# Kernel optimization log

Hardware: AMD Instinct MI355X
Metric: run time of the kernel (lower is better)

The kernel has to match this reference:

```python
import jax, jax.numpy as jnp
import numpy as np

EPS = 1e-8
N_ITERS = 3
LN_EPS = 1e-5  # torch LayerNorm default


def layer_norm(x, g, b):
    mu = jnp.mean(x, axis=-1, keepdims=True)
    var = jnp.var(x, axis=-1, keepdims=True)
    return (x - mu) / jnp.sqrt(var + LN_EPS) * g + b


def setup_inputs() -> dict:
    key = jax.random.key(0)
    ks = jax.random.split(key, 12)
    B, S, F, D_in, D_slot, D_kvq, D_hid = 64, 16, 4096, 512, 512, 512, 2048
    p = lambda i, shape: jax.random.normal(ks[i], shape, dtype=jnp.float32) * 0.02
    return dict(
        slots=jax.random.normal(ks[0], (B, S, D_slot), dtype=jnp.float32),
        features=jax.random.normal(ks[1], (B, F, D_in), dtype=jnp.float32),
        ln_feat_g=jnp.ones((D_in,), jnp.float32), ln_feat_b=jnp.zeros((D_in,), jnp.float32),
        ln_slot_g=jnp.ones((D_slot,), jnp.float32), ln_slot_b=jnp.zeros((D_slot,), jnp.float32),
        w_k=p(2, (D_kvq, D_in)), w_v=p(3, (D_kvq, D_in)), w_q=p(4, (D_kvq, D_slot)),
        gru_w_ih=p(5, (3 * D_slot, D_kvq)), gru_w_hh=p(6, (3 * D_slot, D_slot)),
        gru_b_ih=jnp.zeros((3 * D_slot,), jnp.float32), gru_b_hh=jnp.zeros((3 * D_slot,), jnp.float32),
        mlp_ln_g=jnp.ones((D_slot,), jnp.float32), mlp_ln_b=jnp.zeros((D_slot,), jnp.float32),
        mlp_w1=p(7, (D_hid, D_slot)), mlp_b1=jnp.zeros((D_hid,), jnp.float32),
        mlp_w2=p(8, (D_slot, D_hid)), mlp_b2=jnp.zeros((D_slot,), jnp.float32),
    )


def reference(slots, features, ln_feat_g, ln_feat_b, ln_slot_g, ln_slot_b,
              w_k, w_v, w_q, gru_w_ih, gru_w_hh, gru_b_ih, gru_b_hh,
              mlp_ln_g, mlp_ln_b, mlp_w1, mlp_b1, mlp_w2, mlp_b2):
    scale = w_q.shape[0] ** -0.5  # kvq_dim**-0.5

    f = layer_norm(features, ln_feat_g, ln_feat_b)  # [B,F,D_in]
    keys = f @ w_k.T    # [B,F,D_kvq]
    values = f @ w_v.T  # [B,F,D_kvq]

    def gru_cell(x, h):  # torch.nn.GRUCell semantics
        gi = x @ gru_w_ih.T + gru_b_ih
        gh = h @ gru_w_hh.T + gru_b_hh
        i_r, i_z, i_n = jnp.split(gi, 3, axis=-1)
        h_r, h_z, h_n = jnp.split(gh, 3, axis=-1)
        r = jax.nn.sigmoid(i_r + h_r)
        z = jax.nn.sigmoid(i_z + h_z)
        n = jnp.tanh(i_n + r * h_n)
        return (1.0 - z) * n + z * h

    pre_norm_attn = None
    for _ in range(N_ITERS):  # fixed small iteration count (n_iters=3)
        s_n = layer_norm(slots, ln_slot_g, ln_slot_b)  # note: GRU hidden uses normed slots, per source
        q = s_n @ w_q.T                                 # [B,S,D_kvq]
        dots = jnp.einsum('bsd,bfd->bsf', q, keys) * scale
        pre_norm_attn = jax.nn.softmax(dots, axis=1)    # softmax over SLOT dim
        attn = pre_norm_attn + EPS
        attn = attn / jnp.sum(attn, axis=-1, keepdims=True)
        updates = jnp.einsum('bsf,bfd->bsd', attn, values)
        slots = gru_cell(updates, s_n)
        # residual MLP with initial LayerNorm
        h = layer_norm(slots, mlp_ln_g, mlp_ln_b)
        h = jax.nn.relu(h @ mlp_w1.T + mlp_b1) @ mlp_w2.T + mlp_b2
        slots = slots + h
    return slots, pre_norm_attn
```

## Files before the change

### kernel.cpp

```cpp
#include <hip/hip_runtime.h>


typedef __bf16 bf16x8 __attribute__((ext_vector_type(8)));
typedef float  f32x4  __attribute__((ext_vector_type(4)));

#define DEV static __device__ __forceinline__

DEV float bf2f_lo(unsigned int u) { union { unsigned int i; float f; } v; v.i = u << 16; return v.f; }
DEV unsigned short f2bf(float f) {
  union { float f; unsigned int i; } v; v.f = f;
  return (unsigned short)((v.i + 0x7FFFu + ((v.i >> 16) & 1u)) >> 16);
}

template<int OUTF>
__global__ __launch_bounds__(256) void ln512_kernel(
    const float* __restrict__ X, const float* __restrict__ g,
    const float* __restrict__ b, unsigned short* __restrict__ Yb,
    float* __restrict__ Yf, int R) {
  int wave = (blockIdx.x << 2) | (threadIdx.x >> 6);
  int lane = threadIdx.x & 63;
  if (wave >= R) return;
  const float4* xp = reinterpret_cast<const float4*>(X + (size_t)wave * 512);
  float4 x0 = xp[lane * 2], x1 = xp[lane * 2 + 1];
  float xv[8] = {x0.x, x0.y, x0.z, x0.w, x1.x, x1.y, x1.z, x1.w};
  float s = 0.f, q = 0.f;
#pragma unroll
  for (int j = 0; j < 8; ++j) { s += xv[j]; q += xv[j] * xv[j]; }
#pragma unroll
  for (int off = 32; off; off >>= 1) { s += __shfl_xor(s, off); q += __shfl_xor(q, off); }
  float mu = s * (1.0f / 512.0f);
  float var = q * (1.0f / 512.0f) - mu * mu;
  float rstd = rsqrtf(var + 1e-5f);
  const float4* gp = reinterpret_cast<const float4*>(g);
  const float4* bp = reinterpret_cast<const float4*>(b);
  float4 g0 = gp[lane * 2], g1 = gp[lane * 2 + 1];
  float4 b0 = bp[lane * 2], b1 = bp[lane * 2 + 1];
  float gv[8] = {g0.x, g0.y, g0.z, g0.w, g1.x, g1.y, g1.z, g1.w};
  float bv[8] = {b0.x, b0.y, b0.z, b0.w, b1.x, b1.y, b1.z, b1.w};
  float y[8];
  unsigned short u[8];
#pragma unroll
  for (int j = 0; j < 8; ++j) { y[j] = (xv[j] - mu) * rstd * gv[j] + bv[j]; u[j] = f2bf(y[j]); }
  uint4 o = make_uint4(
      (unsigned)u[0] | ((unsigned)u[1] << 16), (unsigned)u[2] | ((unsigned)u[3] << 16),
      (unsigned)u[4] | ((unsigned)u[5] << 16), (unsigned)u[6] | ((unsigned)u[7] << 16));
  reinterpret_cast<uint4*>(Yb + (size_t)wave * 512)[lane] = o;
  if (OUTF) {
    float4* yf = reinterpret_cast<float4*>(Yf + (size_t)wave * 512);
    yf[lane * 2]     = make_float4(y[0], y[1], y[2], y[3]);
    yf[lane * 2 + 1] = make_float4(y[4], y[5], y[6], y[7]);
  }
}

__global__ __launch_bounds__(256) void prep_weights_kernel(
    const float* __restrict__ w_ih, const float* __restrict__ w_hh,
    const float* __restrict__ w1, const float* __restrict__ w2,
    const float* __restrict__ w_k, const float* __restrict__ w_q,
    const float* __restrict__ w_v,
    unsigned short* __restrict__ Wih, unsigned short* __restrict__ Whh,
    unsigned short* __restrict__ W1, unsigned short* __restrict__ W2,
    unsigned short* __restrict__ WkT, unsigned short* __restrict__ WqT,
    unsigned short* __restrict__ WvT) {
  int blk = blockIdx.x, tid = threadIdx.x;
  if (blk < 3584) {
    const float* src; unsigned short* dst; int base;
    if (blk < 768)       { src = w_ih; dst = Wih; base = blk; }
    else if (blk < 1536) { src = w_hh; dst = Whh; base = blk - 768; }
    else if (blk < 2560) { src = w1;   dst = W1;  base = blk - 1536; }
    else                 { src = w2;   dst = W2;  base = blk - 2560; }
    int i = base * 256 + tid;
    float4 v = reinterpret_cast<const float4*>(src)[i];
    unsigned int lo = (unsigned)f2bf(v.x) | ((unsigned)f2bf(v.y) << 16);
    unsigned int hi = (unsigned)f2bf(v.z) | ((unsigned)f2bf(v.w) << 16);
    reinterpret_cast<uint2*>(dst)[i] = make_uint2(lo, hi);
  } else {
    int rgn = (blk - 3584) >> 10, base = (blk - 3584) & 1023;
    const float* src = rgn == 0 ? w_k : rgn == 1 ? w_q : w_v;
    unsigned short* dst = rgn == 0 ? WkT : rgn == 1 ? WqT : WvT;
    int t2 = base * 256 + tid;
    int i = t2 >> 9, j = t2 & 511;
    dst[t2] = f2bf(src[j * 512 + i]);
  }
}

template<int MODE>
__global__ __launch_bounds__(256) void gemm_nt(
    const unsigned short* __restrict__ A, const unsigned short* __restrict__ Bm,
    const float* __restrict__ bias, unsigned short* __restrict__ Cb,
    int M, int N, int K) {
  int lane = threadIdx.x & 63;
  int w = threadIdx.x >> 6;
  int m0 = blockIdx.y << 5;
  int n0 = (blockIdx.x << 7) + (w << 5);
  int lo = lane & 15, hi = lane >> 4;
  const unsigned short* Ap = A + (size_t)(m0 + lo) * K + (hi << 3);
  const unsigned short* Bp = Bm + (size_t)(n0 + lo) * K + (hi << 3);
  f32x4 acc[2][2];
#pragma unroll
  for (int i = 0; i < 2; ++i)
#pragma unroll
    for (int j = 0; j < 2; ++j) acc[i][j] = f32x4{0.f, 0.f, 0.f, 0.f};
#pragma unroll 2
  for (int kk = 0; kk < K; kk += 32) {
    bf16x8 a0 = *reinterpret_cast<const bf16x8*>(Ap + kk);
    bf16x8 a1 = *reinterpret_cast<const bf16x8*>(Ap + (size_t)16 * K + kk);
    bf16x8 b0 = *reinterpret_cast<const bf16x8*>(Bp + kk);
    bf16x8 b1 = *reinterpret_cast<const bf16x8*>(Bp + (size_t)16 * K + kk);
    acc[0][0] = __builtin_amdgcn_mfma_f32_16x16x32_bf16(a0, b0, acc[0][0], 0, 0, 0);
    acc[0][1] = __builtin_amdgcn_mfma_f32_16x16x32_bf16(a0, b1, acc[0][1], 0, 0, 0);
    acc[1][0] = __builtin_amdgcn_mfma_f32_16x16x32_bf16(a1, b0, acc[1][0], 0, 0, 0);
    acc[1][1] = __builtin_amdgcn_mfma_f32_16x16x32_bf16(a1, b1, acc[1][1], 0, 0, 0);
  }
#pragma unroll
  for (int i = 0; i < 2; ++i)
#pragma unroll
    for (int j = 0; j < 2; ++j) {
      int col = n0 + (j << 4) + lo;
      float bvv = (MODE == 3) ? bias[col] : 0.f;
#pragma unroll
      for (int r = 0; r < 4; ++r) {
        int row = m0 + (i << 4) + (hi << 2) + r;
        float v = acc[i][j][r];
        if (MODE == 0) Cb[(size_t)row * N + col] = f2bf(v);
        else           Cb[(size_t)row * N + col] = f2bf(fmaxf(v + bvv, 0.f));
      }
    }
}

template<int MODE>
__global__ __launch_bounds__(256) void gemm_nt64(
    const unsigned short* __restrict__ A, const unsigned short* __restrict__ Bm,
    const float* __restrict__ bias, const float* __restrict__ res,
    float* __restrict__ Cf, unsigned short* __restrict__ Cb,
    int M, int N, int K) {
  int lane = threadIdx.x & 63;
  int w = threadIdx.x >> 6;
  int m0 = (blockIdx.y << 5) + ((w >> 1) << 4);
  int n0 = (blockIdx.x << 6) + ((w & 1) << 5);
  int lo = lane & 15, hi = lane >> 4;
  const unsigned short* Ap = A + (size_t)(m0 + lo) * K + (hi << 3);
  const unsigned short* Bp = Bm + (size_t)(n0 + lo) * K + (hi << 3);
  f32x4 acc[2];
  acc[0] = f32x4{0.f, 0.f, 0.f, 0.f};
  acc[1] = f32x4{0.f, 0.f, 0.f, 0.f};
#pragma unroll 2
  for (int kk = 0; kk < K; kk += 32) {
    bf16x8 a0 = *reinterpret_cast<const bf16x8*>(Ap + kk);
    bf16x8 b0 = *reinterpret_cast<const bf16x8*>(Bp + kk);
    bf16x8 b1 = *reinterpret_cast<const bf16x8*>(Bp + (size_t)16 * K + kk);
    acc[0] = __builtin_amdgcn_mfma_f32_16x16x32_bf16(a0, b0, acc[0], 0, 0, 0);
    acc[1] = __builtin_amdgcn_mfma_f32_16x16x32_bf16(a0, b1, acc[1], 0, 0, 0);
  }
#pragma unroll
  for (int j = 0; j < 2; ++j) {
    int col = n0 + (j << 4) + lo;
    float bvv = (MODE == 4) ? bias[col] : 0.f;
#pragma unroll
    for (int r = 0; r < 4; ++r) {
      int row = m0 + (hi << 2) + r;
      float v = acc[j][r];
      if (MODE == 0) Cb[(size_t)row * N + col] = f2bf(v);
      else Cf[(size_t)row * N + col] = v + bvv + res[(size_t)row * N + col];
    }
  }
}

__global__ __launch_bounds__(128) void fused_attn_kernel(
    const unsigned short* __restrict__ Qp,
    const unsigned short* __restrict__ Fn,
    float* __restrict__ Upart,
    float* __restrict__ fsumP,
    float* __restrict__ attn_out) {
  __shared__ unsigned short tile[32 * 514];
  __shared__ unsigned short attn_lds[16 * 34];
  int b = blockIdx.y, g = blockIdx.x;
  int t = threadIdx.x;
  int w = t >> 6, lane = t & 63;
  int lo = lane & 15, hi = lane >> 4;
  unsigned int* tile32 = reinterpret_cast<unsigned int*>(tile);

  const unsigned short* qa = Qp + ((size_t)b * 16 + lo) * 512 + (hi << 3);
  const unsigned short* gstage = Fn + ((size_t)b * 4096 + g * 256) * 512;

  f32x4 uacc[16];
#pragma unroll
  for (int s = 0; s < 16; ++s) uacc[s] = f32x4{0.f, 0.f, 0.f, 0.f};
  float fs[4] = {0.f, 0.f, 0.f, 0.f};

  const float scale = 0.04419417382415922f;

  {
    uint4 nx[16];
#pragma unroll
    for (int k = 0; k < 16; ++k)
      nx[k] = *reinterpret_cast<const uint4*>(gstage + (size_t)t * 8 + k * 1024);
#pragma unroll
    for (int k = 0; k < 16; ++k) {
      unsigned int* p32 = tile32 + (k * 2 + w) * 257 + lane * 4;
      p32[0] = nx[k].x; p32[1] = nx[k].y; p32[2] = nx[k].z; p32[3] = nx[k].w;
    }
  }
  __syncthreads();

  for (int c = 0; c < 8; ++c) {
    uint4 nx[16];
    if (c < 7) {
      const unsigned short* src = gstage + (size_t)(c + 1) * 16384;
#pragma unroll
      for (int k = 0; k < 16; ++k)
        nx[k] = *reinterpret_cast<const uint4*>(src + (size_t)t * 8 + k * 1024);
    }
    f32x4 dacc = {0.f, 0.f, 0.f, 0.f};
#pragma unroll
    for (int ks = 0; ks < 16; ++ks) {
      const unsigned int* bp32 = tile32 + (w * 16 + lo) * 257 + ks * 16 + (hi << 2);
      union { unsigned int u[4]; bf16x8 v; } bf;
      bf.u[0] = bp32[0]; bf.u[1] = bp32[1]; bf.u[2] = bp32[2]; bf.u[3] = bp32[3];
      bf16x8 a = *reinterpret_cast<const bf16x8*>(qa + ks * 32);
      dacc = __builtin_amdgcn_mfma_f32_16x16x32_bf16(a, bf.v, dacc, 0, 0, 0);
    }
    float d4[4], mx = -3.4e38f;
#pragma unroll
    for (int r = 0; r < 4; ++r) { d4[r] = dacc[r] * scale; mx = fmaxf(mx, d4[r]); }
    mx = fmaxf(mx, __shfl_xor(mx, 16));
    mx = fmaxf(mx, __shfl_xor(mx, 32));
    float e4[4], ss = 0.f;
#pragma unroll
    for (int r = 0; r < 4; ++r) { e4[r] = __expf(d4[r] - mx); ss += e4[r]; }
    ss += __shfl_xor(ss, 16);
    ss += __shfl_xor(ss, 32);
    float inv = 1.f / ss;
    float cs[4];
#pragma unroll
    for (int r = 0; r < 4; ++r) {
      float p = e4[r] * inv;
      if (attn_out)
        attn_out[((size_t)b * 16 + (hi << 2) + r) * 4096 + g * 256 + c * 32 + (w << 4) + lo] = p;
      unsigned short uu = f2bf(p + 1e-8f);
      attn_lds[((hi << 2) + r) * 34 + (w << 4) + lo] = uu;
      cs[r] = bf2f_lo(uu);
    }
#pragma unroll
    for (int m = 1; m < 16; m <<= 1) {
#pragma unroll
      for (int r = 0; r < 4; ++r) cs[r] += __shfl_xor(cs[r], m);
    }
#pragma unroll
    for (int r = 0; r < 4; ++r) fs[r] += cs[r];
    __syncthreads();
    {
      const unsigned int* ap32 = reinterpret_cast<const unsigned int*>(attn_lds) + lo * 17 + (hi << 2);
      union { unsigned int u[4]; bf16x8 v; } paf;
      paf.u[0] = ap32[0]; paf.u[1] = ap32[1]; paf.u[2] = ap32[2]; paf.u[3] = ap32[3];
#pragma unroll
      for (int sub = 0; sub < 16; ++sub) {
        int dcol = (w << 8) + (sub << 4) + lo;
        union { unsigned short u[8]; bf16x8 v; } pbf;
#pragma unroll
        for (int j = 0; j < 8; ++j)
          pbf.u[j] = tile[((hi << 3) + j) * 514 + dcol];
        uacc[sub] = __builtin_amdgcn_mfma_f32_16x16x32_bf16(paf.v, pbf.v, uacc[sub], 0, 0, 0);
      }
    }
    __syncthreads();
    if (c < 7) {
#pragma unroll
      for (int k = 0; k < 16; ++k) {
        unsigned int* p32 = tile32 + (k * 2 + w) * 257 + lane * 4;
        p32[0] = nx[k].x; p32[1] = nx[k].y; p32[2] = nx[k].z; p32[3] = nx[k].w;
      }
      __syncthreads();
    }
  }
#pragma unroll
  for (int sub = 0; sub < 16; ++sub) {
#pragma unroll
    for (int r = 0; r < 4; ++r)
      Upart[((size_t)(b * 16 + g) * 16 + (hi << 2) + r) * 512 + (w << 8) + (sub << 4) + lo] = uacc[sub][r];
  }
  if (lo == 0) {
#pragma unroll
    for (int r = 0; r < 4; ++r)
      fsumP[((size_t)(b * 16 + g) * 2 + w) * 16 + (hi << 2) + r] = fs[r];
  }
}

__global__ __launch_bounds__(256) void upd_fin_kernel(
    const float* __restrict__ Upart, const float* __restrict__ fsumP,
    unsigned short* __restrict__ outb) {
  int blk = blockIdx.x;
  int b = blk >> 5;
  int s = (blk >> 1) & 15;
  int d = ((blk & 1) << 8) + threadIdx.x;
  float fsum = 0.f;
#pragma unroll
  for (int i = 0; i < 32; ++i) fsum += fsumP[(size_t)b * 512 + i * 16 + s];
  float inv = 1.f / fsum;
  const float* p = Upart + (size_t)b * 131072 + s * 512 + d;
  float acc = 0.f;
#pragma unroll
  for (int g = 0; g < 16; ++g) acc += p[(size_t)g * 8192];
  outb[((size_t)b * 16 + s) * 512 + d] = f2bf(acc * inv);
}

__global__ __launch_bounds__(256) void gru_gemm_kernel(
    const unsigned short* __restrict__ Au, const unsigned short* __restrict__ As,
    const unsigned short* __restrict__ Wc2, const unsigned short* __restrict__ Whh,
    const float* __restrict__ b_ih, const float* __restrict__ b_hh,
    const float* __restrict__ snf, float* __restrict__ hout) {
  int lane = threadIdx.x & 63, w = threadIdx.x >> 6;
  int lo = lane & 15, hi = lane >> 4;
  int m0 = blockIdx.y << 4;
  int cw = (blockIdx.x << 7) + (w << 5);
  const unsigned short* aup = Au + (size_t)(m0 + lo) * 512 + (hi << 3);
  const unsigned short* asp = As + (size_t)(m0 + lo) * 512 + (hi << 3);
  const unsigned short* bc[2][3];
  const unsigned short* bh[2][3];
#pragma unroll
  for (int jt = 0; jt < 2; ++jt)
#pragma unroll
    for (int gt = 0; gt < 3; ++gt) {
      size_t rowoff = (size_t)(cw + jt * 16 + gt * 512 + lo) * 512 + (hi << 3);
      bc[jt][gt] = Wc2 + rowoff;
      bh[jt][gt] = Whh + rowoff;
    }
  f32x4 gi[2][3], gh[2][3];
#pragma unroll
  for (int jt = 0; jt < 2; ++jt)
#pragma unroll
    for (int gt = 0; gt < 3; ++gt) {
      gi[jt][gt] = f32x4{0.f, 0.f, 0.f, 0.f};
      gh[jt][gt] = f32x4{0.f, 0.f, 0.f, 0.f};
    }
  for (int kk = 0; kk < 512; kk += 32) {
    bf16x8 au = *reinterpret_cast<const bf16x8*>(aup + kk);
    bf16x8 as_ = *reinterpret_cast<const bf16x8*>(asp + kk);
#pragma unroll
    for (int jt = 0; jt < 2; ++jt)
#pragma unroll
      for (int gt = 0; gt < 3; ++gt) {
        bf16x8 wc = *reinterpret_cast<const bf16x8*>(bc[jt][gt] + kk);
        bf16x8 wh = *reinterpret_cast<const bf16x8*>(bh[jt][gt] + kk);
        gi[jt][gt] = __builtin_amdgcn_mfma_f32_16x16x32_bf16(au, wc, gi[jt][gt], 0, 0, 0);
        gh[jt][gt] = __builtin_amdgcn_mfma_f32_16x16x32_bf16(as_, wh, gh[jt][gt], 0, 0, 0);
      }
  }
#pragma unroll
  for (int jt = 0; jt < 2; ++jt) {
    int col = cw + (jt << 4) + lo;
    float bir = b_ih[col], biz = b_ih[col + 512], bin = b_ih[col + 1024];
    float bhr = b_hh[col], bhz = b_hh[col + 512], bhn = b_hh[col + 1024];
#pragma unroll
    for (int r = 0; r < 4; ++r) {
      int row = m0 + (hi << 2) + r;
      float rr = (gi[jt][0][r] + bir) + (gh[jt][0][r] + bhr);
      float zz = (gi[jt][1][r] + biz) + (gh[jt][1][r] + bhz);
      float rg = 1.f / (1.f + __expf(-rr));
      float zg = 1.f / (1.f + __expf(-zz));
      float a = (gi[jt][2][r] + bin) + rg * (gh[jt][2][r] + bhn);
      float ee = __expf(-2.f * fabsf(a));
      float nt = (1.f - ee) / (1.f + ee);
      float n = copysignf(nt, a);
      float hp = snf[(size_t)row * 512 + col];
      hout[(size_t)row * 512 + col] = (1.f - zg) * n + zg * hp;
    }
  }
}

extern "C" void kernel_launch(void* const* d_in, const int* in_sizes, int n_in,
                              void* d_out, int out_size, void* d_ws, size_t ws_size,
                              hipStream_t stream) {
  const float* slots_in  = (const float*)d_in[0];
  const float* features  = (const float*)d_in[1];
  const float* ln_feat_g = (const float*)d_in[2];
  const float* ln_feat_b = (const float*)d_in[3];
  const float* ln_slot_g = (const float*)d_in[4];
  const float* ln_slot_b = (const float*)d_in[5];
  const float* w_k  = (const float*)d_in[6];
  const float* w_v  = (const float*)d_in[7];
  const float* w_q  = (const float*)d_in[8];
  const float* w_ih = (const float*)d_in[9];
  const float* w_hh = (const float*)d_in[10];
  const float* b_ih = (const float*)d_in[11];
  const float* b_hh = (const float*)d_in[12];
  const float* mlp_ln_g = (const float*)d_in[13];
  const float* mlp_ln_b = (const float*)d_in[14];
  const float* w1 = (const float*)d_in[15];
  const float* b1 = (const float*)d_in[16];
  const float* w2 = (const float*)d_in[17];
  const float* b2 = (const float*)d_in[18];

  char* ws = (char*)d_ws;
  size_t off = 0;
  auto alloc = [&](size_t bytes) {
    char* p = ws + off;
    off += (bytes + 255) & ~(size_t)255;
    return p;
  };
  unsigned short* f_norm  = (unsigned short*)alloc((size_t)64 * 4096 * 512 * 2);
  unsigned short* qp_bf   = (unsigned short*)alloc(1024 * 512 * 2);
  float*          s_n_f   = (float*)alloc(1024 * 512 * 4);
  unsigned short* s_n_bf  = (unsigned short*)alloc(1024 * 512 * 2);
  float*          fsumP   = (float*)alloc(64 * 32 * 16 * 4);
  float*          Upart   = (float*)alloc((size_t)64 * 16 * 16 * 512 * 4);
  unsigned short* updp_bf = (unsigned short*)alloc(1024 * 512 * 2);
  float*          slots_c = (float*)alloc(1024 * 512 * 4);
  unsigned short* hln_bf  = (unsigned short*)alloc(1024 * 512 * 2);
  unsigned short* hm_bf   = (unsigned short*)alloc((size_t)1024 * 2048 * 2);
  unsigned short* Wqk_bf  = (unsigned short*)alloc(512 * 512 * 2);
  unsigned short* Wih_bf  = (unsigned short*)alloc(1536 * 512 * 2);
  unsigned short* Whh_bf  = (unsigned short*)alloc(1536 * 512 * 2);
  unsigned short* WkT_bf  = (unsigned short*)alloc(512 * 512 * 2);
  unsigned short* WqT_bf  = (unsigned short*)alloc(512 * 512 * 2);
  unsigned short* WvT_bf  = (unsigned short*)alloc(512 * 512 * 2);
  unsigned short* Wc2_bf  = (unsigned short*)alloc(1536 * 512 * 2);
  unsigned short* W1_bf   = (unsigned short*)alloc((size_t)2048 * 512 * 2);
  unsigned short* W2_bf   = (unsigned short*)alloc((size_t)512 * 2048 * 2);

  float* out_slots = (float*)d_out;
  float* out_attn  = out_slots + 1024 * 512;

  prep_weights_kernel<<<dim3(6656), dim3(256), 0, stream>>>(
      w_ih, w_hh, w1, w2, w_k, w_q, w_v,
      Wih_bf, Whh_bf, W1_bf, W2_bf, WkT_bf, WqT_bf, WvT_bf);
  gemm_nt<0><<<dim3(4, 16), dim3(256), 0, stream>>>(
      WkT_bf, WqT_bf, nullptr, Wqk_bf, 512, 512, 512);
  gemm_nt<0><<<dim3(4, 48), dim3(256), 0, stream>>>(
      Wih_bf, WvT_bf, nullptr, Wc2_bf, 1536, 512, 512);
  ln512_kernel<0><<<dim3(65536), dim3(256), 0, stream>>>(
      features, ln_feat_g, ln_feat_b, f_norm, nullptr, 262144);

  for (int it = 0; it < 3; ++it) {
    const float* slots_src = (it == 0) ? slots_in : slots_c;
    ln512_kernel<1><<<dim3(256), dim3(256), 0, stream>>>(
        slots_src, ln_slot_g, ln_slot_b, s_n_bf, s_n_f, 1024);
    gemm_nt64<0><<<dim3(8, 32), dim3(256), 0, stream>>>(
        s_n_bf, Wqk_bf, nullptr, nullptr, nullptr, qp_bf, 1024, 512, 512);
    fused_attn_kernel<<<dim3(16, 64), dim3(128), 0, stream>>>(
        qp_bf, f_norm, Upart, fsumP, (it == 2) ? out_attn : nullptr);
    upd_fin_kernel<<<dim3(2048), dim3(256), 0, stream>>>(Upart, fsumP, updp_bf);
    gru_gemm_kernel<<<dim3(4, 64), dim3(256), 0, stream>>>(
        updp_bf, s_n_bf, Wc2_bf, Whh_bf, b_ih, b_hh, s_n_f, slots_c);
    ln512_kernel<0><<<dim3(256), dim3(256), 0, stream>>>(
        slots_c, mlp_ln_g, mlp_ln_b, hln_bf, nullptr, 1024);
    gemm_nt<3><<<dim3(16, 32), dim3(256), 0, stream>>>(
        hln_bf, W1_bf, b1, hm_bf, 1024, 2048, 512);
    float* slot_dst = (it == 2) ? out_slots : slots_c;
    gemm_nt64<4><<<dim3(8, 32), dim3(256), 0, stream>>>(
        hm_bf, W2_bf, b2, slots_c, slot_dst, nullptr, 1024, 512, 2048);
  }
  (void)in_sizes; (void)n_in; (void)out_size; (void)ws_size;
}
```

Baseline: 694.7 us.

## Fuse partial-update reduction into GRU GEMM and LayerNorm into MLP first GEMM

Removes the standalone upd_fin kernel: each GRU GEMM block now reduces the Upart partials and fsum for its batch itself, normalises them, and stages the bf16 update rows in padded LDS. It also fuses the MLP LayerNorm into a new ln_mlp1 kernel that normalises 32 rows into LDS before the W1 GEMM with bias+ReLU. This cuts two kernel launches per iteration and the intermediate bf16 round trips through global memory. The cost is redundant work: the reduction is repeated by each of the 4 column blocks, and the LayerNorm by each of the 16 column blocks.

```diff
diff --git a/kernel.cpp b/kernel.cpp
--- a/kernel.cpp
+++ b/kernel.cpp
@@ -116,13 +116,10 @@
 #pragma unroll
     for (int j = 0; j < 2; ++j) {
       int col = n0 + (j << 4) + lo;
-      float bvv = (MODE == 3) ? bias[col] : 0.f;
 #pragma unroll
       for (int r = 0; r < 4; ++r) {
         int row = m0 + (i << 4) + (hi << 2) + r;
-        float v = acc[i][j][r];
-        if (MODE == 0) Cb[(size_t)row * N + col] = f2bf(v);
-        else           Cb[(size_t)row * N + col] = f2bf(fmaxf(v + bvv, 0.f));
+        Cb[(size_t)row * N + col] = f2bf(acc[i][j][r]);
       }
     }
 }
@@ -285,34 +282,46 @@
   }
 }
 
-__global__ __launch_bounds__(256) void upd_fin_kernel(
-    const float* __restrict__ Upart, const float* __restrict__ fsumP,
-    unsigned short* __restrict__ outb) {
-  int blk = blockIdx.x;
-  int b = blk >> 5;
-  int s = (blk >> 1) & 15;
-  int d = ((blk & 1) << 8) + threadIdx.x;
-  float fsum = 0.f;
-#pragma unroll
-  for (int i = 0; i < 32; ++i) fsum += fsumP[(size_t)b * 512 + i * 16 + s];
-  float inv = 1.f / fsum;
-  const float* p = Upart + (size_t)b * 131072 + s * 512 + d;
-  float acc = 0.f;
-#pragma unroll
-  for (int g = 0; g < 16; ++g) acc += p[(size_t)g * 8192];
-  outb[((size_t)b * 16 + s) * 512 + d] = f2bf(acc * inv);
-}
-
 __global__ __launch_bounds__(256) void gru_gemm_kernel(
-    const unsigned short* __restrict__ Au, const unsigned short* __restrict__ As,
-    const unsigned short* __restrict__ Wc2, const unsigned short* __restrict__ Whh,
+    const float* __restrict__ Upart,
+    const float* __restrict__ fsumP,
+    const unsigned short* __restrict__ As,
+    const unsigned short* __restrict__ Wc2,
+    const unsigned short* __restrict__ Whh,
     const float* __restrict__ b_ih, const float* __restrict__ b_hh,
-    const float* __restrict__ snf, float* __restrict__ hout) {
-  int lane = threadIdx.x & 63, w = threadIdx.x >> 6;
+    const float* __restrict__ snf,
+    float* __restrict__ hout) {
+  __shared__ unsigned int au_lds[16 * 261];
+  int b = blockIdx.y;
+  int t = threadIdx.x;
+  {
+    int s = t & 15;
+    int dchunk = (t >> 4) << 5;
+    float fsum = 0.f;
+#pragma unroll
+    for (int i = 0; i < 32; ++i) fsum += fsumP[(size_t)b * 512 + i * 16 + s];
+    float inv = 1.f / fsum;
+    const float* p = Upart + (size_t)b * 131072 + s * 512 + dchunk;
+#pragma unroll
+    for (int q = 0; q < 8; ++q) {
+      float4 acc = make_float4(0.f, 0.f, 0.f, 0.f);
+#pragma unroll
+      for (int g = 0; g < 16; ++g) {
+        float4 v = *reinterpret_cast<const float4*>(p + (size_t)g * 8192 + q * 4);
+        acc.x += v.x; acc.y += v.y; acc.z += v.z; acc.w += v.w;
+      }
+      unsigned int w0 = (unsigned)f2bf(acc.x * inv) | ((unsigned)f2bf(acc.y * inv) << 16);
+      unsigned int w1 = (unsigned)f2bf(acc.z * inv) | ((unsigned)f2bf(acc.w * inv) << 16);
+      unsigned int* dst = au_lds + s * 261 + ((dchunk + q * 4) >> 1);
+      dst[0] = w0; dst[1] = w1;
+    }
+  }
+  __syncthreads();
+  int lane = t & 63, w = t >> 6;
   int lo = lane & 15, hi = lane >> 4;
-  int m0 = blockIdx.y << 4;
+  int m0 = b << 4;
   int cw = (blockIdx.x << 7) + (w << 5);
-  const unsigned short* aup = Au + (size_t)(m0 + lo) * 512 + (hi << 3);
+  const unsigned int* aup32 = au_lds + lo * 261 + (hi << 2);
   const unsigned short* asp = As + (size_t)(m0 + lo) * 512 + (hi << 3);
   const unsigned short* bc[2][3];
   const unsigned short* bh[2][3];
@@ -333,7 +342,9 @@
       gh[jt][gt] = f32x4{0.f, 0.f, 0.f, 0.f};
     }
   for (int kk = 0; kk < 512; kk += 32) {
-    bf16x8 au = *reinterpret_cast<const bf16x8*>(aup + kk);
+    union { unsigned int u[4]; bf16x8 v; } au;
+    const unsigned int* ap = aup32 + (kk >> 1);
+    au.u[0] = ap[0]; au.u[1] = ap[1]; au.u[2] = ap[2]; au.u[3] = ap[3];
     bf16x8 as_ = *reinterpret_cast<const bf16x8*>(asp + kk);
 #pragma unroll
     for (int jt = 0; jt < 2; ++jt)
@@ -341,7 +352,7 @@
       for (int gt = 0; gt < 3; ++gt) {
         bf16x8 wc = *reinterpret_cast<const bf16x8*>(bc[jt][gt] + kk);
         bf16x8 wh = *reinterpret_cast<const bf16x8*>(bh[jt][gt] + kk);
-        gi[jt][gt] = __builtin_amdgcn_mfma_f32_16x16x32_bf16(au, wc, gi[jt][gt], 0, 0, 0);
+        gi[jt][gt] = __builtin_amdgcn_mfma_f32_16x16x32_bf16(au.v, wc, gi[jt][gt], 0, 0, 0);
         gh[jt][gt] = __builtin_amdgcn_mfma_f32_16x16x32_bf16(as_, wh, gh[jt][gt], 0, 0, 0);
       }
   }
@@ -365,6 +376,85 @@
       hout[(size_t)row * 512 + col] = (1.f - zg) * n + zg * hp;
     }
   }
+}
+
+__global__ __launch_bounds__(256) void ln_mlp1_kernel(
+    const float* __restrict__ X,
+    const float* __restrict__ g, const float* __restrict__ bta,
+    const unsigned short* __restrict__ W1,
+    const float* __restrict__ b1,
+    unsigned short* __restrict__ hm) {
+  __shared__ unsigned int lds[32 * 261];
+  int m0 = blockIdx.y << 5;
+  int t = threadIdx.x, w = t >> 6, lane = t & 63;
+  {
+    const float4* gp = reinterpret_cast<const float4*>(g) + lane * 2;
+    const float4* bp = reinterpret_cast<const float4*>(bta) + lane * 2;
+    float4 g0 = gp[0], g1 = gp[1], c0 = bp[0], c1 = bp[1];
+    float gv[8] = {g0.x, g0.y, g0.z, g0.w, g1.x, g1.y, g1.z, g1.w};
+    float bv[8] = {c0.x, c0.y, c0.z, c0.w, c1.x, c1.y, c1.z, c1.w};
+#pragma unroll
+    for (int p = 0; p < 8; ++p) {
+      int r = (p << 2) | w;
+      const float4* xp = reinterpret_cast<const float4*>(X + (size_t)(m0 + r) * 512) + lane * 2;
+      float4 x0 = xp[0], x1 = xp[1];
+      float xv[8] = {x0.x, x0.y, x0.z, x0.w, x1.x, x1.y, x1.z, x1.w};
+      float s = 0.f, q = 0.f;
+#pragma unroll
+      for (int j = 0; j < 8; ++j) { s += xv[j]; q += xv[j] * xv[j]; }
+#pragma unroll
+      for (int off = 32; off; off >>= 1) { s += __shfl_xor(s, off); q += __shfl_xor(q, off); }
+      float mu = s * (1.0f / 512.0f);
+      float var = q * (1.0f / 512.0f) - mu * mu;
+      float rstd = rsqrtf(var + 1e-5f);
+      unsigned int pk[4];
+#pragma unroll
+      for (int j = 0; j < 4; ++j) {
+        unsigned short u0 = f2bf((xv[2 * j] - mu) * rstd * gv[2 * j] + bv[2 * j]);
+        unsigned short u1 = f2bf((xv[2 * j + 1] - mu) * rstd * gv[2 * j + 1] + bv[2 * j + 1]);
+        pk[j] = (unsigned)u0 | ((unsigned)u1 << 16);
+      }
+      unsigned int* dst = lds + r * 261 + lane * 4;
+      dst[0] = pk[0]; dst[1] = pk[1]; dst[2] = pk[2]; dst[3] = pk[3];
+    }
+  }
+  __syncthreads();
+  int lo = lane & 15, hi = lane >> 4;
+  int n0 = (blockIdx.x << 7) + (w << 5);
+  const unsigned short* Bp = W1 + (size_t)(n0 + lo) * 512 + (hi << 3);
+  f32x4 acc[2][2];
+#pragma unroll
+  for (int i = 0; i < 2; ++i)
+#pragma unroll
+    for (int j = 0; j < 2; ++j) acc[i][j] = f32x4{0.f, 0.f, 0.f, 0.f};
+  const unsigned int* a0p = lds + lo * 261 + (hi << 2);
+  const unsigned int* a1p = lds + (16 + lo) * 261 + (hi << 2);
+#pragma unroll 2
+  for (int kk = 0; kk < 512; kk += 32) {
+    union { unsigned int u[4]; bf16x8 v; } a0, a1;
+    const unsigned int* p0 = a0p + (kk >> 1);
+    const unsigned int* p1 = a1p + (kk >> 1);
+    a0.u[0] = p0[0]; a0.u[1] = p0[1]; a0.u[2] = p0[2]; a0.u[3] = p0[3];
+    a1.u[0] = p1[0]; a1.u[1] = p1[1]; a1.u[2] = p1[2]; a1.u[3] = p1[3];
+    bf16x8 b0 = *reinterpret_cast<const bf16x8*>(Bp + kk);
+    bf16x8 b1 = *reinterpret_cast<const bf16x8*>(Bp + (size_t)16 * 512 + kk);
+    acc[0][0] = __builtin_amdgcn_mfma_f32_16x16x32_bf16(a0.v, b0, acc[0][0], 0, 0, 0);
+    acc[0][1] = __builtin_amdgcn_mfma_f32_16x16x32_bf16(a0.v, b1, acc[0][1], 0, 0, 0);
+    acc[1][0] = __builtin_amdgcn_mfma_f32_16x16x32_bf16(a1.v, b0, acc[1][0], 0, 0, 0);
+    acc[1][1] = __builtin_amdgcn_mfma_f32_16x16x32_bf16(a1.v, b1, acc[1][1], 0, 0, 0);
+  }
+#pragma unroll
+  for (int i = 0; i < 2; ++i)
+#pragma unroll
+    for (int j = 0; j < 2; ++j) {
+      int col = n0 + (j << 4) + lo;
+      float bvv = b1[col];
+#pragma unroll
+      for (int r = 0; r < 4; ++r) {
+        int row = m0 + (i << 4) + (hi << 2) + r;
+        hm[(size_t)row * 2048 + col] = f2bf(fmaxf(acc[i][j][r] + bvv, 0.f));
+      }
+    }
 }
 
 extern "C" void kernel_launch(void* const* d_in, const int* in_sizes, int n_in,
@@ -403,9 +493,7 @@
   unsigned short* s_n_bf  = (unsigned short*)alloc(1024 * 512 * 2);
   float*          fsumP   = (float*)alloc(64 * 32 * 16 * 4);
   float*          Upart   = (float*)alloc((size_t)64 * 16 * 16 * 512 * 4);
-  unsigned short* updp_bf = (unsigned short*)alloc(1024 * 512 * 2);
   float*          slots_c = (float*)alloc(1024 * 512 * 4);
-  unsigned short* hln_bf  = (unsigned short*)alloc(1024 * 512 * 2);
   unsigned short* hm_bf   = (unsigned short*)alloc((size_t)1024 * 2048 * 2);
   unsigned short* Wqk_bf  = (unsigned short*)alloc(512 * 512 * 2);
   unsigned short* Wih_bf  = (unsigned short*)alloc(1536 * 512 * 2);
@@ -438,13 +526,10 @@
         s_n_bf, Wqk_bf, nullptr, nullptr, nullptr, qp_bf, 1024, 512, 512);
     fused_attn_kernel<<<dim3(16, 64), dim3(128), 0, stream>>>(
         qp_bf, f_norm, Upart, fsumP, (it == 2) ? out_attn : nullptr);
-    upd_fin_kernel<<<dim3(2048), dim3(256), 0, stream>>>(Upart, fsumP, updp_bf);
     gru_gemm_kernel<<<dim3(4, 64), dim3(256), 0, stream>>>(
-        updp_bf, s_n_bf, Wc2_bf, Whh_bf, b_ih, b_hh, s_n_f, slots_c);
-    ln512_kernel<0><<<dim3(256), dim3(256), 0, stream>>>(
-        slots_c, mlp_ln_g, mlp_ln_b, hln_bf, nullptr, 1024);
-    gemm_nt<3><<<dim3(16, 32), dim3(256), 0, stream>>>(
-        hln_bf, W1_bf, b1, hm_bf, 1024, 2048, 512);
+        Upart, fsumP, s_n_bf, Wc2_bf, Whh_bf, b_ih, b_hh, s_n_f, slots_c);
+    ln_mlp1_kernel<<<dim3(16, 32), dim3(256), 0, stream>>>(
+        slots_c, mlp_ln_g, mlp_ln_b, W1_bf, b1, hm_bf);
     float* slot_dst = (it == 2) ? out_slots : slots_c;
     gemm_nt64<4><<<dim3(8, 32), dim3(256), 0, stream>>>(
         hm_bf, W2_bf, b2, slots_c, slot_dst, nullptr, 1024, 512, 2048);
```

Result: slower. 755.2 us (+8.7%).
